# Kernel tuning notes

Measured on AMD Instinct MI355X. Metric: run time of the kernel, lower is better.

Reference implementation:

```python
import jax, jax.numpy as jnp
import numpy as np

T = 2.0          # hardcoded in __init__ (self.T = 2)
EPSILON = 0.1    # sinkhorn_loss default
N_ITERS = 10     # sinkhorn_loss default passed to sinkhorn_normalized
COST_CLIP = 10.0
TINY = 1e-8

B, S, V = 16, 512, 4096


def setup_inputs() -> dict:
    key = jax.random.key(0)
    k1, k2 = jax.random.split(key)
    y_s = jax.random.normal(k1, (B, S, V), dtype=jnp.float32)
    y_t = jax.random.normal(k2, (B, S, V), dtype=jnp.float32)
    return {"y_s": y_s, "y_t": y_t}


def _cdist_l1(x, y):
    # x, y: [S, V] -> [S, S]; row-streamed via lax.map to avoid a [S,S,V] intermediate
    return jax.lax.map(lambda xi: jnp.sum(jnp.abs(xi[None, :] - y), axis=-1), x)


def _sinkhorn_loss(x, y):
    # x, y: [S, V] softmax probabilities for one sample
    Wxy = _cdist_l1(x, y)                                  # [S, S]
    K = jnp.exp(-jnp.minimum(Wxy, COST_CLIP) / EPSILON)
    P = jnp.nan_to_num(K, nan=TINY, posinf=1e6, neginf=-1e6) + TINY
    for _ in range(N_ITERS):
        P = P / jnp.maximum(jnp.sum(P, axis=1, keepdims=True), TINY)
        P = jnp.nan_to_num(P, nan=TINY)
        P = P / jnp.maximum(jnp.sum(P, axis=0, keepdims=True), TINY)
        P = jnp.nan_to_num(P, nan=TINY)
    return jnp.sum(P * Wxy)


def reference(y_s, y_t):
    p_s = jax.nn.softmax(y_s / T, axis=-1)
    p_t = jax.nn.softmax(y_t / T, axis=-1)
    p_s = jnp.nan_to_num(p_s, nan=TINY)
    p_t = jnp.nan_to_num(p_t, nan=TINY)
    per_sample = jax.vmap(_sinkhorn_loss)(p_s, p_t)        # [B]
    # forward accumulates 0.001 * loss_i and divides by the number of valid samples
    return jnp.mean(0.001 * per_sample)
```

## Files before the change

kernel.cpp:

```cpp
#include <hip/hip_runtime.h>

#define B_ 16
#define S_ 512
#define V_ 4096

typedef unsigned int uint;
typedef unsigned short ushort;
typedef unsigned char u8;


__device__ __forceinline__ uint sad8(uint a, uint b, uint c) {
#if __has_builtin(__builtin_amdgcn_sad_u8)
    return __builtin_amdgcn_sad_u8(a, b, c);
#else
    uint s = c;
#pragma unroll
    for (int i = 0; i < 4; ++i) {
        uint x = (a >> (8 * i)) & 0xFFu, y = (b >> (8 * i)) & 0xFFu;
        s += x > y ? x - y : y - x;
    }
    return s;
#endif
}

__device__ __forceinline__ float bflo(uint p) { return __uint_as_float(p << 16); }
__device__ __forceinline__ float bfhi(uint p) { return __uint_as_float(p & 0xFFFF0000u); }

__device__ __forceinline__ ushort f2bf(float f) {
    uint u = __float_as_uint(f);
    u = (u + 0x7FFFu + ((u >> 16) & 1u)) >> 16;
    return (ushort)u;
}

__device__ __forceinline__ float waveMax(float v) {
#pragma unroll
    for (int o = 32; o; o >>= 1) v = fmaxf(v, __shfl_xor(v, o, 64));
    return v;
}
__device__ __forceinline__ float waveSum(float v) {
#pragma unroll
    for (int o = 32; o; o >>= 1) v += __shfl_xor(v, o, 64);
    return v;
}

#define GLOAD_LDS16(g, l)                                                      \
    __builtin_amdgcn_global_load_lds(                                          \
        (const __attribute__((address_space(1))) uint*)(g),                    \
        (__attribute__((address_space(3))) uint*)(l), 16, 0, 0)

#define QSCALE 65536.0f
#define QINV   1.52587890625e-5f

__global__ __launch_bounds__(256) void softmax_kernel(
        const float* __restrict__ ys, const float* __restrict__ yt,
        u8* __restrict__ qs, u8* __restrict__ qt) {
    const int row = blockIdx.x;
    const float* in = blockIdx.y ? yt : ys;
    u8* out = blockIdx.y ? qt : qs;
    const float* px = in + (size_t)row * V_;
    u8* po = out + (size_t)row * V_;
    const int tid = threadIdx.x;

    float4 v4[4];
    float m = -3.4e38f;
#pragma unroll
    for (int i = 0; i < 4; ++i) {
        v4[i] = ((const float4*)px)[tid + 256 * i];
        m = fmaxf(m, fmaxf(fmaxf(v4[i].x, v4[i].y), fmaxf(v4[i].z, v4[i].w)));
    }
    __shared__ float redm[4], reds[4];
    float wm = waveMax(m);
    if ((tid & 63) == 0) redm[tid >> 6] = wm;
    __syncthreads();
    const float rm = fmaxf(fmaxf(redm[0], redm[1]), fmaxf(redm[2], redm[3]));

    float e[16];
    float s = 0.f;
#pragma unroll
    for (int i = 0; i < 4; ++i) {
        const float* f = (const float*)&v4[i];
#pragma unroll
        for (int k = 0; k < 4; ++k) {
            float ev = __expf((f[k] - rm) * 0.5f);
            e[i * 4 + k] = ev;
            s += ev;
        }
    }
    float wsm = waveSum(s);
    if ((tid & 63) == 0) reds[tid >> 6] = wsm;
    __syncthreads();
    const float inv = 1.0f / (reds[0] + reds[1] + reds[2] + reds[3]);

#pragma unroll
    for (int i = 0; i < 4; ++i) {
        uint pk = 0;
#pragma unroll
        for (int k = 0; k < 4; ++k) {
            float p = e[i * 4 + k] * inv;
            uint q = (uint)fminf(p * QSCALE + 0.5f, 255.f);
            pk |= q << (8 * k);
        }
        ((uint*)po)[tid + 256 * i] = pk;
    }
}

#define TI 128
#define TJ 128
#define KCB 64

__global__ __launch_bounds__(256) void pairwise_kernel(
        const u8* __restrict__ qs, const u8* __restrict__ qt,
        uint* __restrict__ Acc) {
    const int bz = blockIdx.z;
    const int b = bz >> 2, vq = bz & 3;
    const int tR = blockIdx.y * TI;
    const int tC = blockIdx.x * TJ;
    const u8* xrow = qs + (size_t)b * S_ * V_ + vq * (V_ / 4) + (size_t)tR * V_;
    const u8* yrow = qt + (size_t)b * S_ * V_ + vq * (V_ / 4) + (size_t)tC * V_;
    const int tid = threadIdx.x;
    const int lane = tid & 63, wv = tid >> 6;
    const int tx = tid & 15, ty = tid >> 4;

    __shared__ u8 xs[2][TI * KCB];
    __shared__ u8 ysm[2][TJ * KCB];

    const int rs = lane >> 2;
    const int coff = (((lane & 3) ^ ((lane >> 3) & 3)) << 4);
    const size_t gs0 = (size_t)((wv * 2) * 16 + rs) * V_ + coff;
    const size_t gs1 = (size_t)((wv * 2 + 1) * 16 + rs) * V_ + coff;
    const int ls0 = (wv * 2) * 1024;
    const int ls1 = (wv * 2 + 1) * 1024;

    uint acc[8][8];
#pragma unroll
    for (int r = 0; r < 8; ++r)
#pragma unroll
        for (int c = 0; c < 8; ++c) acc[r][c] = 0u;

    GLOAD_LDS16(xrow + gs0, &xs[0][ls0]);
    GLOAD_LDS16(xrow + gs1, &xs[0][ls1]);
    GLOAD_LDS16(yrow + gs0, &ysm[0][ls0]);
    GLOAD_LDS16(yrow + gs1, &ysm[0][ls1]);
    __syncthreads();

    for (int c0 = 0; c0 < (V_ / 4) / KCB; ++c0) {
        const int cur = c0 & 1;
        if (c0 + 1 < (V_ / 4) / KCB) {
            const int kn = (c0 + 1) * KCB;
            GLOAD_LDS16(xrow + kn + gs0, &xs[cur ^ 1][ls0]);
            GLOAD_LDS16(xrow + kn + gs1, &xs[cur ^ 1][ls1]);
            GLOAD_LDS16(yrow + kn + gs0, &ysm[cur ^ 1][ls0]);
            GLOAD_LDS16(yrow + kn + gs1, &ysm[cur ^ 1][ls1]);
        }
#pragma unroll
        for (int kk = 0; kk < 4; ++kk) {
            uint4 Af[8], Bf[8];
#pragma unroll
            for (int r = 0; r < 8; ++r) {
                const int R = ty + 16 * r;
                Af[r] = *(const uint4*)
                    &xs[cur][R * KCB + ((kk ^ ((R >> 1) & 3)) << 4)];
            }
#pragma unroll
            for (int c = 0; c < 8; ++c) {
                const int C = tx + 16 * c;
                Bf[c] = *(const uint4*)
                    &ysm[cur][C * KCB + ((kk ^ ((C >> 1) & 3)) << 4)];
            }
#pragma unroll
            for (int r = 0; r < 8; ++r)
#pragma unroll
                for (int c = 0; c < 8; ++c) {
                    uint t = sad8(Af[r].x, Bf[c].x, acc[r][c]);
                    t = sad8(Af[r].y, Bf[c].y, t);
                    t = sad8(Af[r].z, Bf[c].z, t);
                    acc[r][c] = sad8(Af[r].w, Bf[c].w, t);
                }
        }
        __syncthreads();
    }

#pragma unroll
    for (int r = 0; r < 8; ++r) {
        const int i = tR + ty + 16 * r;
        const size_t base = ((size_t)b * S_ + i) * S_;
#pragma unroll
        for (int c = 0; c < 8; ++c) {
            const int j = tC + tx + 16 * c;
            atomicAdd(&Acc[base + j], acc[r][c]);
        }
    }
}

__global__ __launch_bounds__(256) void pairwise_epi(
        const uint* __restrict__ Acc, ushort* __restrict__ Wb,
        ushort* __restrict__ Kb) {
    const size_t g = (size_t)blockIdx.x * 256 + threadIdx.x;
    uint4 a = ((const uint4*)Acc)[g];
    union { uint2 u; ushort h[4]; } pw, pk;
    uint av[4] = {a.x, a.y, a.z, a.w};
#pragma unroll
    for (int t = 0; t < 4; ++t) {
        float w = fminf((float)av[t] * QINV, 10.f);
        pw.h[t] = f2bf(w);
        pk.h[t] = f2bf(__expf(-10.f * w) + 1e-8f);
    }
    ((uint2*)Wb)[g] = pw.u;
    ((uint2*)Kb)[g] = pk.u;
}

__global__ __launch_bounds__(1024) void sink_block(
        const ushort* __restrict__ Kb, const ushort* __restrict__ Wb,
        float* __restrict__ out) {
    const int b = blockIdx.x;
    const int tid = threadIdx.x, lane = tid & 63, wv = tid >> 6;
    const int ch = lane & 31, rq = lane >> 5;

    __shared__ float vp[S_];
    __shared__ float uls[S_];
    __shared__ float cwp[16][S_];
    __shared__ float redw[16];

    if (tid < S_) { vp[tid] = 1.f; uls[tid] = 1.f; }
    __syncthreads();

    const ushort* Kl = Kb + (size_t)b * S_ * S_;
    const int chB = ch * 16;

    for (int it = 0; it < 10; ++it) {
        const float4 v0 = *(const float4*)&vp[chB];
        const float4 v1 = *(const float4*)&vp[chB + 4];
        const float4 v2 = *(const float4*)&vp[chB + 8];
        const float4 v3 = *(const float4*)&vp[chB + 12];
        float4 c0 = make_float4(0.f, 0.f, 0.f, 0.f);
        float4 c1 = c0, c2 = c0, c3 = c0;

#pragma unroll 2
        for (int g = 0; g < 16; ++g) {
            const int i = wv * 32 + g * 2 + rq;
            const ushort* kp = Kl + (size_t)i * S_ + chB;
            const uint4 ka = *(const uint4*)kp;
            const uint4 kc = *(const uint4*)(kp + 8);
            float d0 = 0.f, d1 = 0.f;
            d0 = fmaf(bflo(ka.x), v0.x, d0); d0 = fmaf(bfhi(ka.x), v0.y, d0);
            d0 = fmaf(bflo(ka.y), v0.z, d0); d0 = fmaf(bfhi(ka.y), v0.w, d0);
            d0 = fmaf(bflo(ka.z), v1.x, d0); d0 = fmaf(bfhi(ka.z), v1.y, d0);
            d0 = fmaf(bflo(ka.w), v1.z, d0); d0 = fmaf(bfhi(ka.w), v1.w, d0);
            d1 = fmaf(bflo(kc.x), v2.x, d1); d1 = fmaf(bfhi(kc.x), v2.y, d1);
            d1 = fmaf(bflo(kc.y), v2.z, d1); d1 = fmaf(bfhi(kc.y), v2.w, d1);
            d1 = fmaf(bflo(kc.z), v3.x, d1); d1 = fmaf(bfhi(kc.z), v3.y, d1);
            d1 = fmaf(bflo(kc.w), v3.z, d1); d1 = fmaf(bfhi(kc.w), v3.w, d1);
            float dot = d0 + d1;
            dot += __shfl_xor(dot, 1, 64);
            dot += __shfl_xor(dot, 2, 64);
            dot += __shfl_xor(dot, 4, 64);
            dot += __shfl_xor(dot, 8, 64);
            dot += __shfl_xor(dot, 16, 64);
            const float up = uls[i];
            const float un = up / fmaxf(up * dot, 1e-8f);
            if (ch == 0) uls[i] = un;
            c0.x = fmaf(un, bflo(ka.x), c0.x); c0.y = fmaf(un, bfhi(ka.x), c0.y);
            c0.z = fmaf(un, bflo(ka.y), c0.z); c0.w = fmaf(un, bfhi(ka.y), c0.w);
            c1.x = fmaf(un, bflo(ka.z), c1.x); c1.y = fmaf(un, bfhi(ka.z), c1.y);
            c1.z = fmaf(un, bflo(ka.w), c1.z); c1.w = fmaf(un, bfhi(ka.w), c1.w);
            c2.x = fmaf(un, bflo(kc.x), c2.x); c2.y = fmaf(un, bfhi(kc.x), c2.y);
            c2.z = fmaf(un, bflo(kc.y), c2.z); c2.w = fmaf(un, bfhi(kc.y), c2.w);
            c3.x = fmaf(un, bflo(kc.z), c3.x); c3.y = fmaf(un, bfhi(kc.z), c3.y);
            c3.z = fmaf(un, bflo(kc.w), c3.z); c3.w = fmaf(un, bfhi(kc.w), c3.w);
        }
        c0.x += __shfl_xor(c0.x, 32, 64); c0.y += __shfl_xor(c0.y, 32, 64);
        c0.z += __shfl_xor(c0.z, 32, 64); c0.w += __shfl_xor(c0.w, 32, 64);
        c1.x += __shfl_xor(c1.x, 32, 64); c1.y += __shfl_xor(c1.y, 32, 64);
        c1.z += __shfl_xor(c1.z, 32, 64); c1.w += __shfl_xor(c1.w, 32, 64);
        c2.x += __shfl_xor(c2.x, 32, 64); c2.y += __shfl_xor(c2.y, 32, 64);
        c2.z += __shfl_xor(c2.z, 32, 64); c2.w += __shfl_xor(c2.w, 32, 64);
        c3.x += __shfl_xor(c3.x, 32, 64); c3.y += __shfl_xor(c3.y, 32, 64);
        c3.z += __shfl_xor(c3.z, 32, 64); c3.w += __shfl_xor(c3.w, 32, 64);
        if (rq == 0) {
            *(float4*)&cwp[wv][chB] = c0;
            *(float4*)&cwp[wv][chB + 4] = c1;
        } else {
            *(float4*)&cwp[wv][chB + 8] = c2;
            *(float4*)&cwp[wv][chB + 12] = c3;
        }
        __syncthreads();
        if (tid < S_) {
            float s = 0.f;
#pragma unroll
            for (int t = 0; t < 16; ++t) s += cwp[t][tid];
            const float vv = vp[tid];
            vp[tid] = vv / fmaxf(vv * s, 1e-8f);
        }
        __syncthreads();
    }

    const float4 v0 = *(const float4*)&vp[chB];
    const float4 v1 = *(const float4*)&vp[chB + 4];
    const float4 v2 = *(const float4*)&vp[chB + 8];
    const float4 v3 = *(const float4*)&vp[chB + 12];
    const ushort* Wl = Wb + (size_t)b * S_ * S_;
    float accl = 0.f;
#pragma unroll 2
    for (int g = 0; g < 16; ++g) {
        const int i = wv * 32 + g * 2 + rq;
        const ushort* kp = Kl + (size_t)i * S_ + chB;
        const ushort* wp = Wl + (size_t)i * S_ + chB;
        const uint4 ka = *(const uint4*)kp;
        const uint4 kc = *(const uint4*)(kp + 8);
        const uint4 wa = *(const uint4*)wp;
        const uint4 wc = *(const uint4*)(wp + 8);
        float r0 = 0.f, r1 = 0.f;
        r0 = fmaf(bflo(ka.x) * v0.x, bflo(wa.x), r0);
        r0 = fmaf(bfhi(ka.x) * v0.y, bfhi(wa.x), r0);
        r0 = fmaf(bflo(ka.y) * v0.z, bflo(wa.y), r0);
        r0 = fmaf(bfhi(ka.y) * v0.w, bfhi(wa.y), r0);
        r0 = fmaf(bflo(ka.z) * v1.x, bflo(wa.z), r0);
        r0 = fmaf(bfhi(ka.z) * v1.y, bfhi(wa.z), r0);
        r0 = fmaf(bflo(ka.w) * v1.z, bflo(wa.w), r0);
        r0 = fmaf(bfhi(ka.w) * v1.w, bfhi(wa.w), r0);
        r1 = fmaf(bflo(kc.x) * v2.x, bflo(wc.x), r1);
        r1 = fmaf(bfhi(kc.x) * v2.y, bfhi(wc.x), r1);
        r1 = fmaf(bflo(kc.y) * v2.z, bflo(wc.y), r1);
        r1 = fmaf(bfhi(kc.y) * v2.w, bfhi(wc.y), r1);
        r1 = fmaf(bflo(kc.z) * v3.x, bflo(wc.z), r1);
        r1 = fmaf(bfhi(kc.z) * v3.y, bfhi(wc.z), r1);
        r1 = fmaf(bflo(kc.w) * v3.z, bflo(wc.w), r1);
        r1 = fmaf(bfhi(kc.w) * v3.w, bfhi(wc.w), r1);
        float rp = r0 + r1;
        rp += __shfl_xor(rp, 1, 64);
        rp += __shfl_xor(rp, 2, 64);
        rp += __shfl_xor(rp, 4, 64);
        rp += __shfl_xor(rp, 8, 64);
        rp += __shfl_xor(rp, 16, 64);
        if (ch == 0) accl = fmaf(uls[i], rp, accl);
    }
    accl += __shfl_xor(accl, 32, 64);
    if (lane == 0) redw[wv] = accl;
    __syncthreads();
    if (tid == 0) {
        float s = 0.f;
#pragma unroll
        for (int t = 0; t < 16; ++t) s += redw[t];
        atomicAdd(out, s * (0.001f / 16.f));
    }
}

extern "C" void kernel_launch(void* const* d_in, const int* in_sizes, int n_in,
                              void* d_out, int out_size, void* d_ws, size_t ws_size,
                              hipStream_t stream) {
    const float* ys = (const float*)d_in[0];
    const float* yt = (const float*)d_in[1];
    float* out = (float*)d_out;

    char* w = (char*)d_ws;
    u8* qs = (u8*)w;
    u8* qt = qs + (size_t)B_ * S_ * V_;
    uint* Acc = (uint*)(qt + (size_t)B_ * S_ * V_);
    ushort* Wb = (ushort*)qs;
    ushort* Kb = Wb + (size_t)B_ * S_ * S_;

    (void)hipMemsetAsync(Acc, 0, (size_t)B_ * S_ * S_ * 4, stream);
    (void)hipMemsetAsync(out, 0, sizeof(float), stream);

    softmax_kernel<<<dim3(8192, 2), 256, 0, stream>>>(ys, yt, qs, qt);
    pairwise_kernel<<<dim3(4, 4, 64), 256, 0, stream>>>(qs, qt, Acc);
    pairwise_epi<<<4096, 256, 0, stream>>>(Acc, Wb, Kb);
    sink_block<<<16, 1024, 0, stream>>>(Kb, Wb, out);
}
```

Baseline: 548.8 us.

## Drop split-K atomics and fuse cost/kernel epilogue into pairwise SAD kernel

Replaces the split-K pairwise L1 kernel (4 V-quarters accumulated via atomicAdd into a uint buffer, then a separate epilogue) with a full-K kernel using 64x64 tiles that writes bf16 W and K directly. This removes the accumulator memset, the global atomics and one extra kernel pass over a 16 MB buffer. In exchange each thread holds a 4x4 accumulator instead of 8x8, so fewer SAD ops are done per LDS load, and the final stores are scalar 16-bit writes.

```diff
diff --git a/kernel.cpp b/kernel.cpp
--- a/kernel.cpp
+++ b/kernel.cpp
@@ -104,19 +104,18 @@
     }
 }
 
-#define TI 128
-#define TJ 128
+#define TI 64
+#define TJ 64
 #define KCB 64
 
 __global__ __launch_bounds__(256) void pairwise_kernel(
         const u8* __restrict__ qs, const u8* __restrict__ qt,
-        uint* __restrict__ Acc) {
-    const int bz = blockIdx.z;
-    const int b = bz >> 2, vq = bz & 3;
+        ushort* __restrict__ Wb, ushort* __restrict__ Kb) {
+    const int b = blockIdx.z;
     const int tR = blockIdx.y * TI;
     const int tC = blockIdx.x * TJ;
-    const u8* xrow = qs + (size_t)b * S_ * V_ + vq * (V_ / 4) + (size_t)tR * V_;
-    const u8* yrow = qt + (size_t)b * S_ * V_ + vq * (V_ / 4) + (size_t)tC * V_;
+    const u8* xrow = qs + (size_t)b * S_ * V_ + (size_t)tR * V_;
+    const u8* yrow = qt + (size_t)b * S_ * V_ + (size_t)tC * V_;
     const int tid = threadIdx.x;
     const int lane = tid & 63, wv = tid >> 6;
     const int tx = tid & 15, ty = tid >> 4;
@@ -126,51 +125,46 @@
 
     const int rs = lane >> 2;
     const int coff = (((lane & 3) ^ ((lane >> 3) & 3)) << 4);
-    const size_t gs0 = (size_t)((wv * 2) * 16 + rs) * V_ + coff;
-    const size_t gs1 = (size_t)((wv * 2 + 1) * 16 + rs) * V_ + coff;
-    const int ls0 = (wv * 2) * 1024;
-    const int ls1 = (wv * 2 + 1) * 1024;
-
-    uint acc[8][8];
-#pragma unroll
-    for (int r = 0; r < 8; ++r)
-#pragma unroll
-        for (int c = 0; c < 8; ++c) acc[r][c] = 0u;
-
-    GLOAD_LDS16(xrow + gs0, &xs[0][ls0]);
-    GLOAD_LDS16(xrow + gs1, &xs[0][ls1]);
-    GLOAD_LDS16(yrow + gs0, &ysm[0][ls0]);
-    GLOAD_LDS16(yrow + gs1, &ysm[0][ls1]);
-    __syncthreads();
-
-    for (int c0 = 0; c0 < (V_ / 4) / KCB; ++c0) {
+    const size_t gsrc = (size_t)(wv * 16 + rs) * V_ + coff;
+    const int ldst = wv * 1024;
+
+    uint acc[4][4];
+#pragma unroll
+    for (int r = 0; r < 4; ++r)
+#pragma unroll
+        for (int c = 0; c < 4; ++c) acc[r][c] = 0u;
+
+    GLOAD_LDS16(xrow + gsrc, &xs[0][ldst]);
+    GLOAD_LDS16(yrow + gsrc, &ysm[0][ldst]);
+    __syncthreads();
+
+#pragma unroll 2
+    for (int c0 = 0; c0 < V_ / KCB; ++c0) {
         const int cur = c0 & 1;
-        if (c0 + 1 < (V_ / 4) / KCB) {
-            const int kn = (c0 + 1) * KCB;
-            GLOAD_LDS16(xrow + kn + gs0, &xs[cur ^ 1][ls0]);
-            GLOAD_LDS16(xrow + kn + gs1, &xs[cur ^ 1][ls1]);
-            GLOAD_LDS16(yrow + kn + gs0, &ysm[cur ^ 1][ls0]);
-            GLOAD_LDS16(yrow + kn + gs1, &ysm[cur ^ 1][ls1]);
+        if (c0 + 1 < V_ / KCB) {
+            const size_t kn = (size_t)(c0 + 1) * KCB;
+            GLOAD_LDS16(xrow + kn + gsrc, &xs[cur ^ 1][ldst]);
+            GLOAD_LDS16(yrow + kn + gsrc, &ysm[cur ^ 1][ldst]);
         }
 #pragma unroll
         for (int kk = 0; kk < 4; ++kk) {
-            uint4 Af[8], Bf[8];
-#pragma unroll
-            for (int r = 0; r < 8; ++r) {
+            uint4 Af[4], Bf[4];
+#pragma unroll
+            for (int r = 0; r < 4; ++r) {
                 const int R = ty + 16 * r;
                 Af[r] = *(const uint4*)
                     &xs[cur][R * KCB + ((kk ^ ((R >> 1) & 3)) << 4)];
             }
 #pragma unroll
-            for (int c = 0; c < 8; ++c) {
+            for (int c = 0; c < 4; ++c) {
                 const int C = tx + 16 * c;
                 Bf[c] = *(const uint4*)
                     &ysm[cur][C * KCB + ((kk ^ ((C >> 1) & 3)) << 4)];
             }
 #pragma unroll
-            for (int r = 0; r < 8; ++r)
-#pragma unroll
-                for (int c = 0; c < 8; ++c) {
+            for (int r = 0; r < 4; ++r)
+#pragma unroll
+                for (int c = 0; c < 4; ++c) {
                     uint t = sad8(Af[r].x, Bf[c].x, acc[r][c]);
                     t = sad8(Af[r].y, Bf[c].y, t);
                     t = sad8(Af[r].z, Bf[c].z, t);
@@ -181,32 +175,17 @@
     }
 
 #pragma unroll
-    for (int r = 0; r < 8; ++r) {
+    for (int r = 0; r < 4; ++r) {
         const int i = tR + ty + 16 * r;
         const size_t base = ((size_t)b * S_ + i) * S_;
 #pragma unroll
-        for (int c = 0; c < 8; ++c) {
+        for (int c = 0; c < 4; ++c) {
             const int j = tC + tx + 16 * c;
-            atomicAdd(&Acc[base + j], acc[r][c]);
-        }
-    }
-}
-
-__global__ __launch_bounds__(256) void pairwise_epi(
-        const uint* __restrict__ Acc, ushort* __restrict__ Wb,
-        ushort* __restrict__ Kb) {
-    const size_t g = (size_t)blockIdx.x * 256 + threadIdx.x;
-    uint4 a = ((const uint4*)Acc)[g];
-    union { uint2 u; ushort h[4]; } pw, pk;
-    uint av[4] = {a.x, a.y, a.z, a.w};
-#pragma unroll
-    for (int t = 0; t < 4; ++t) {
-        float w = fminf((float)av[t] * QINV, 10.f);
-        pw.h[t] = f2bf(w);
-        pk.h[t] = f2bf(__expf(-10.f * w) + 1e-8f);
-    }
-    ((uint2*)Wb)[g] = pw.u;
-    ((uint2*)Kb)[g] = pk.u;
+            const float w = fminf((float)acc[r][c] * QINV, 10.f);
+            Wb[base + j] = f2bf(w);
+            Kb[base + j] = f2bf(__expf(-10.f * w) + 1e-8f);
+        }
+    }
 }
 
 __global__ __launch_bounds__(1024) void sink_block(
@@ -355,15 +334,12 @@
     char* w = (char*)d_ws;
     u8* qs = (u8*)w;
     u8* qt = qs + (size_t)B_ * S_ * V_;
-    uint* Acc = (uint*)(qt + (size_t)B_ * S_ * V_);
-    ushort* Wb = (ushort*)qs;
+    ushort* Wb = (ushort*)(qt + (size_t)B_ * S_ * V_);
     ushort* Kb = Wb + (size_t)B_ * S_ * S_;
 
-    (void)hipMemsetAsync(Acc, 0, (size_t)B_ * S_ * S_ * 4, stream);
     (void)hipMemsetAsync(out, 0, sizeof(float), stream);
 
     softmax_kernel<<<dim3(8192, 2), 256, 0, stream>>>(ys, yt, qs, qt);
-    pairwise_kernel<<<dim3(4, 4, 64), 256, 0, stream>>>(qs, qt, Acc);
-    pairwise_epi<<<4096, 256, 0, stream>>>(Acc, Wb, Kb);
+    pairwise_kernel<<<dim3(8, 8, 16), 256, 0, stream>>>(qs, qt, Wb, Kb);
     sink_block<<<16, 1024, 0, stream>>>(Kb, Wb, out);
 }
```

After: 543.6 us. Within noise of the previous version (-0.9%).
